# Optimization experiments

Hardware: AMD Instinct MI355X
Metric: run time of the kernel (lower is better)

Reference implementation:

```python
import jax, jax.numpy as jnp
import numpy as np

B = 4096        # graphs per batch
N_PER = 64      # nodes per graph
N = B * N_PER   # total nodes
D = 512         # embed_dim
T = 2048        # target_size


def setup_inputs() -> dict:
    key = jax.random.key(0)
    k1, k2, k3 = jax.random.split(key, 3)
    batch_emb = jax.random.normal(k1, (N, D), dtype=jnp.float32)
    # sorted per-node graph ids (PyG `batch` vector), all graphs non-empty
    seg = jnp.repeat(jnp.arange(B, dtype=jnp.int64), N_PER)
    # local node indices of the two query nodes in each graph
    targets = jax.random.randint(k2, (B, 2), 0, N_PER, dtype=jnp.int64)
    W = jax.random.normal(k3, (T, 3 * D), dtype=jnp.float32) * (1.0 / np.sqrt(3 * D))
    b = jnp.zeros((T,), dtype=jnp.float32)
    return {"batch_emb": batch_emb, "seg": seg, "targets": targets, "W": W, "b": b}


def reference(batch_emb, seg, targets, W, b):
    # per-graph mean pooling (segment mean)
    sums = jax.ops.segment_sum(batch_emb, seg, num_segments=B)          # [B, D]
    counts = jax.ops.segment_sum(jnp.ones((batch_emb.shape[0],), batch_emb.dtype),
                                 seg, num_segments=B)                   # [B]
    node_avg = sums / counts[:, None]                                   # [B, D]
    # convert local query indices to global node indices via segment starts
    starts = jnp.cumsum(counts.astype(jnp.int64)) - counts.astype(jnp.int64)  # [B]
    global_idx = starts[:, None] + targets                              # [B, 2]
    q = batch_emb[global_idx]                                           # [B, 2, D]
    final_embs = jnp.concatenate([q[:, 0], q[:, 1], node_avg], axis=-1) # [B, 3D]
    return final_embs @ W.T + b                                         # [B, T]
```

## Files before the change

kernel.cpp:

```cpp
#include <hip/hip_runtime.h>
#include <hip/hip_bf16.h>
#include <stdint.h>

#define B_GRAPHS 4096
#define N_PER    64
#define D_EMB    512
#define T_OUT    2048
#define K_DIM    1536

typedef __bf16 bf16x8 __attribute__((ext_vector_type(8)));
typedef float  f32x4  __attribute__((ext_vector_type(4)));

__global__ __launch_bounds__(128) void pool_gather_kernel(
    const float* __restrict__ emb, const int* __restrict__ targets,
    __hip_bfloat16* __restrict__ lhs)
{
    const int g = blockIdx.x;
    const int t = threadIdx.x;
    const int t0 = targets[2*g];
    const int t1 = targets[2*g + 1];
    const float4* rows = reinterpret_cast<const float4*>(emb)
                         + (size_t)g * N_PER * (D_EMB/4) + t;
    float4 acc = make_float4(0.f, 0.f, 0.f, 0.f);
    #pragma unroll 16
    for (int n = 0; n < N_PER; ++n) {
        float4 v = rows[(size_t)n * (D_EMB/4)];
        acc.x += v.x; acc.y += v.y; acc.z += v.z; acc.w += v.w;
    }
    const float s = 1.0f / (float)N_PER;
    float4 avg = make_float4(acc.x*s, acc.y*s, acc.z*s, acc.w*s);
    float4 q0 = rows[(size_t)t0 * (D_EMB/4)];
    float4 q1 = rows[(size_t)t1 * (D_EMB/4)];

    __hip_bfloat16* row = lhs + (size_t)g * K_DIM;
    union Pack { __hip_bfloat16 h[4]; uint2 u; };
    Pack p0, p1, pa;
    p0.h[0] = __float2bfloat16(q0.x); p0.h[1] = __float2bfloat16(q0.y);
    p0.h[2] = __float2bfloat16(q0.z); p0.h[3] = __float2bfloat16(q0.w);
    p1.h[0] = __float2bfloat16(q1.x); p1.h[1] = __float2bfloat16(q1.y);
    p1.h[2] = __float2bfloat16(q1.z); p1.h[3] = __float2bfloat16(q1.w);
    pa.h[0] = __float2bfloat16(avg.x); pa.h[1] = __float2bfloat16(avg.y);
    pa.h[2] = __float2bfloat16(avg.z); pa.h[3] = __float2bfloat16(avg.w);
    reinterpret_cast<uint2*>(row)[t]             = p0.u;
    reinterpret_cast<uint2*>(row + D_EMB)[t]     = p1.u;
    reinterpret_cast<uint2*>(row + 2*D_EMB)[t]   = pa.u;
}

__global__ __launch_bounds__(256) void wconv_kernel(
    const float* __restrict__ W, __hip_bfloat16* __restrict__ Wb)
{
    const int i = blockIdx.x * 256 + threadIdx.x;
    const float4 v = reinterpret_cast<const float4*>(W)[i];
    union Pack { __hip_bfloat16 h[4]; uint2 u; } p;
    p.h[0] = __float2bfloat16(v.x); p.h[1] = __float2bfloat16(v.y);
    p.h[2] = __float2bfloat16(v.z); p.h[3] = __float2bfloat16(v.w);
    reinterpret_cast<uint2*>(Wb)[i] = p.u;
}

__global__ __launch_bounds__(256) void gemm_kernel(
    const __hip_bfloat16* __restrict__ A,
    const __hip_bfloat16* __restrict__ Bm,
    const float* __restrict__ bias,
    float* __restrict__ C)
{
    __shared__ __align__(16) __hip_bfloat16 As[128*64];
    __shared__ __align__(16) __hip_bfloat16 Bs[128*64];

    const int tid = threadIdx.x;
    const int w   = tid >> 6;
    const int l   = tid & 63;
    const int wr  = w >> 1;
    const int wc  = w & 1;
    const int brow = blockIdx.y * 128;
    const int bcol = blockIdx.x * 128;

    const int sr   = l >> 3;
    const int scol = 8 * ((l & 7) ^ sr);

    char* AsB = reinterpret_cast<char*>(As);
    char* BsB = reinterpret_cast<char*>(Bs);

    f32x4 acc[4][4];
    #pragma unroll
    for (int m = 0; m < 4; ++m)
        #pragma unroll
        for (int n = 0; n < 4; ++n)
            acc[m][n] = (f32x4){0.f, 0.f, 0.f, 0.f};

    for (int kt = 0; kt < K_DIM/64; ++kt) {
        const int k0 = kt * 64;
        if (kt) __syncthreads();
        #pragma unroll
        for (int c = 0; c < 4; ++c) {
            const int ch = w * 4 + c;
            const int r  = ch * 8 + sr;
            const __hip_bfloat16* ga = A  + (size_t)(brow + r) * K_DIM + k0 + scol;
            const __hip_bfloat16* gb = Bm + (size_t)(bcol + r) * K_DIM + k0 + scol;
            __builtin_amdgcn_global_load_lds(
                (const __attribute__((address_space(1))) void*)ga,
                (__attribute__((address_space(3))) void*)(AsB + ch*1024), 16, 0, 0);
            __builtin_amdgcn_global_load_lds(
                (const __attribute__((address_space(1))) void*)gb,
                (__attribute__((address_space(3))) void*)(BsB + ch*1024), 16, 0, 0);
        }
        __syncthreads();

        #pragma unroll
        for (int kk = 0; kk < 2; ++kk) {
            const int kbyte = kk*64 + (l >> 4)*16;
            bf16x8 af[4], bf[4];
            #pragma unroll
            for (int m = 0; m < 4; ++m) {
                const int r = wr*64 + m*16 + (l & 15);
                af[m] = *reinterpret_cast<const bf16x8*>(
                            AsB + r*128 + (kbyte ^ ((r & 7) << 4)));
            }
            #pragma unroll
            for (int n = 0; n < 4; ++n) {
                const int r = wc*64 + n*16 + (l & 15);
                bf[n] = *reinterpret_cast<const bf16x8*>(
                            BsB + r*128 + (kbyte ^ ((r & 7) << 4)));
            }
            #pragma unroll
            for (int m = 0; m < 4; ++m)
                #pragma unroll
                for (int n = 0; n < 4; ++n)
                    acc[m][n] = __builtin_amdgcn_mfma_f32_16x16x32_bf16(
                                    af[m], bf[n], acc[m][n], 0, 0, 0);
        }
    }

    #pragma unroll
    for (int n = 0; n < 4; ++n) {
        const int col = bcol + wc*64 + n*16 + (l & 15);
        const float bv = bias[col];
        #pragma unroll
        for (int m = 0; m < 4; ++m) {
            const int row0 = brow + wr*64 + m*16 + (l >> 4)*4;
            #pragma unroll
            for (int e = 0; e < 4; ++e) {
                C[(size_t)(row0 + e) * T_OUT + col] = acc[m][n][e] + bv;
            }
        }
    }
}

extern "C" void kernel_launch(void* const* d_in, const int* in_sizes, int n_in,
                              void* d_out, int out_size, void* d_ws, size_t ws_size,
                              hipStream_t stream) {
    const float* emb     = (const float*)d_in[0];
    const int*   targets = (const int*)d_in[2];
    const float* W       = (const float*)d_in[3];
    const float* bias    = (const float*)d_in[4];
    float* out = (float*)d_out;

    __hip_bfloat16* lhs = (__hip_bfloat16*)d_ws;
    __hip_bfloat16* wb  = lhs + (size_t)B_GRAPHS * K_DIM;

    pool_gather_kernel<<<B_GRAPHS, 128, 0, stream>>>(emb, targets, lhs);
    wconv_kernel<<<(T_OUT * K_DIM / 4) / 256, 256, 0, stream>>>(W, wb);
    gemm_kernel<<<dim3(T_OUT/128, B_GRAPHS/128), 256, 0, stream>>>(lhs, wb, bias, out);
}
```

Baseline: 148.7 us.

## Double-buffer GEMM LDS tiles and merge W conversion into pooling kernel

The GEMM now keeps two LDS buffers and issues the asynchronous global-to-LDS loads for the next K tile before computing on the current one. This is meant to hide load latency and drop one barrier per iteration. Separately, the W fp32-to-bf16 conversion is folded into the pooling launch as extra grid-stride blocks, which removes one kernel launch and lets both memory-bound jobs overlap. The cost is doubled LDS per GEMM block (64KB), which may lower occupancy.

```diff
diff --git a/kernel.cpp b/kernel.cpp
--- a/kernel.cpp
+++ b/kernel.cpp
@@ -7,14 +7,33 @@
 #define D_EMB    512
 #define T_OUT    2048
 #define K_DIM    1536
+#define KT_N     (K_DIM/64)
+#define WCONV_BLOCKS 512
 
 typedef __bf16 bf16x8 __attribute__((ext_vector_type(8)));
 typedef float  f32x4  __attribute__((ext_vector_type(4)));
 
-__global__ __launch_bounds__(128) void pool_gather_kernel(
+__global__ __launch_bounds__(128) void pool_conv_kernel(
     const float* __restrict__ emb, const int* __restrict__ targets,
-    __hip_bfloat16* __restrict__ lhs)
+    const float* __restrict__ W,
+    __hip_bfloat16* __restrict__ lhs, __hip_bfloat16* __restrict__ wb)
 {
+    union Pack { __hip_bfloat16 h[4]; uint2 u; };
+
+    if (blockIdx.x >= B_GRAPHS) {
+        const int total = T_OUT * K_DIM / 4;
+        const int nthr  = WCONV_BLOCKS * 128;
+        for (int i = (blockIdx.x - B_GRAPHS) * 128 + threadIdx.x;
+             i < total; i += nthr) {
+            const float4 v = reinterpret_cast<const float4*>(W)[i];
+            Pack p;
+            p.h[0] = __float2bfloat16(v.x); p.h[1] = __float2bfloat16(v.y);
+            p.h[2] = __float2bfloat16(v.z); p.h[3] = __float2bfloat16(v.w);
+            reinterpret_cast<uint2*>(wb)[i] = p.u;
+        }
+        return;
+    }
+
     const int g = blockIdx.x;
     const int t = threadIdx.x;
     const int t0 = targets[2*g];
@@ -33,7 +52,6 @@
     float4 q1 = rows[(size_t)t1 * (D_EMB/4)];
 
     __hip_bfloat16* row = lhs + (size_t)g * K_DIM;
-    union Pack { __hip_bfloat16 h[4]; uint2 u; };
     Pack p0, p1, pa;
     p0.h[0] = __float2bfloat16(q0.x); p0.h[1] = __float2bfloat16(q0.y);
     p0.h[2] = __float2bfloat16(q0.z); p0.h[3] = __float2bfloat16(q0.w);
@@ -46,25 +64,14 @@
     reinterpret_cast<uint2*>(row + 2*D_EMB)[t]   = pa.u;
 }
 
-__global__ __launch_bounds__(256) void wconv_kernel(
-    const float* __restrict__ W, __hip_bfloat16* __restrict__ Wb)
-{
-    const int i = blockIdx.x * 256 + threadIdx.x;
-    const float4 v = reinterpret_cast<const float4*>(W)[i];
-    union Pack { __hip_bfloat16 h[4]; uint2 u; } p;
-    p.h[0] = __float2bfloat16(v.x); p.h[1] = __float2bfloat16(v.y);
-    p.h[2] = __float2bfloat16(v.z); p.h[3] = __float2bfloat16(v.w);
-    reinterpret_cast<uint2*>(Wb)[i] = p.u;
-}
-
 __global__ __launch_bounds__(256) void gemm_kernel(
     const __hip_bfloat16* __restrict__ A,
     const __hip_bfloat16* __restrict__ Bm,
     const float* __restrict__ bias,
     float* __restrict__ C)
 {
-    __shared__ __align__(16) __hip_bfloat16 As[128*64];
-    __shared__ __align__(16) __hip_bfloat16 Bs[128*64];
+    __shared__ __align__(16) __hip_bfloat16 As[2][128*64];
+    __shared__ __align__(16) __hip_bfloat16 Bs[2][128*64];
 
     const int tid = threadIdx.x;
     const int w   = tid >> 6;
@@ -77,9 +84,6 @@
     const int sr   = l >> 3;
     const int scol = 8 * ((l & 7) ^ sr);
 
-    char* AsB = reinterpret_cast<char*>(As);
-    char* BsB = reinterpret_cast<char*>(Bs);
-
     f32x4 acc[4][4];
     #pragma unroll
     for (int m = 0; m < 4; ++m)
@@ -87,24 +91,34 @@
         for (int n = 0; n < 4; ++n)
             acc[m][n] = (f32x4){0.f, 0.f, 0.f, 0.f};
 
-    for (int kt = 0; kt < K_DIM/64; ++kt) {
+    const __hip_bfloat16* gA = A  + (size_t)(brow + w*32 + sr) * K_DIM + scol;
+    const __hip_bfloat16* gB = Bm + (size_t)(bcol + w*32 + sr) * K_DIM + scol;
+
+    auto stage = [&](int buf, int kt) {
         const int k0 = kt * 64;
-        if (kt) __syncthreads();
+        char* AsB = reinterpret_cast<char*>(As[buf]);
+        char* BsB = reinterpret_cast<char*>(Bs[buf]);
         #pragma unroll
         for (int c = 0; c < 4; ++c) {
             const int ch = w * 4 + c;
-            const int r  = ch * 8 + sr;
-            const __hip_bfloat16* ga = A  + (size_t)(brow + r) * K_DIM + k0 + scol;
-            const __hip_bfloat16* gb = Bm + (size_t)(bcol + r) * K_DIM + k0 + scol;
             __builtin_amdgcn_global_load_lds(
-                (const __attribute__((address_space(1))) void*)ga,
+                (const __attribute__((address_space(1))) void*)(gA + (size_t)c*8*K_DIM + k0),
                 (__attribute__((address_space(3))) void*)(AsB + ch*1024), 16, 0, 0);
             __builtin_amdgcn_global_load_lds(
-                (const __attribute__((address_space(1))) void*)gb,
+                (const __attribute__((address_space(1))) void*)(gB + (size_t)c*8*K_DIM + k0),
                 (__attribute__((address_space(3))) void*)(BsB + ch*1024), 16, 0, 0);
         }
-        __syncthreads();
+    };
 
+    stage(0, 0);
+    __syncthreads();
+
+    int cur = 0;
+    for (int kt = 0; kt < KT_N; ++kt) {
+        if (kt + 1 < KT_N) stage(cur ^ 1, kt + 1);
+
+        const char* AsB = reinterpret_cast<const char*>(As[cur]);
+        const char* BsB = reinterpret_cast<const char*>(Bs[cur]);
         #pragma unroll
         for (int kk = 0; kk < 2; ++kk) {
             const int kbyte = kk*64 + (l >> 4)*16;
@@ -127,6 +141,11 @@
                 for (int n = 0; n < 4; ++n)
                     acc[m][n] = __builtin_amdgcn_mfma_f32_16x16x32_bf16(
                                     af[m], bf[n], acc[m][n], 0, 0, 0);
+        }
+
+        if (kt + 1 < KT_N) {
+            __syncthreads();
+            cur ^= 1;
         }
     }
 
@@ -157,7 +176,7 @@
     __hip_bfloat16* lhs = (__hip_bfloat16*)d_ws;
     __hip_bfloat16* wb  = lhs + (size_t)B_GRAPHS * K_DIM;
 
-    pool_gather_kernel<<<B_GRAPHS, 128, 0, stream>>>(emb, targets, lhs);
-    wconv_kernel<<<(T_OUT * K_DIM / 4) / 256, 256, 0, stream>>>(W, wb);
+    pool_conv_kernel<<<B_GRAPHS + WCONV_BLOCKS, 128, 0, stream>>>(
+        emb, targets, W, lhs, wb);
     gemm_kernel<<<dim3(T_OUT/128, B_GRAPHS/128), 256, 0, stream>>>(lhs, wb, bias, out);
 }
```

Result: no change. 151.1 us (+1.7%).
